# Optimization experiments

Hardware: AMD Instinct MI355X
Metric: run time of the kernel (lower is better)

The kernel has to match this reference:

```python
import jax, jax.numpy as jnp
import numpy as np

B, N, F = 4, 1024, 256
AVG_DEG = 16.0


def setup_inputs() -> dict:
    key = jax.random.key(0)
    k1, k2, k3, k4 = jax.random.split(key, 4)
    u = jax.random.uniform(k1, (B, N, N))
    A = (u < AVG_DEG / N).astype(jnp.float32)
    A = jnp.maximum(A, jnp.swapaxes(A, 1, 2))            # symmetric
    A = A * (1.0 - jnp.eye(N, dtype=jnp.float32))        # no self loops (added in forward)
    x = jax.random.normal(k2, (B, N, F), dtype=jnp.float32)
    pos = jax.random.normal(k3, (B, N, 3), dtype=jnp.float32)
    order = jax.random.uniform(k4, (B, N), dtype=jnp.float32)  # 'random' ordering priorities
    node_mask = jnp.ones((B, N), dtype=bool)
    return {"x": x, "adj": A, "pos": pos, "order": order, "node_mask": node_mask}


def _select(order, excluded, included, node_mask):
    # Greedy frontier-based node selection (K-MIS with stride=2).
    Bn, Nn = order.shape
    ar = jnp.arange(Nn)
    idx0 = jnp.argmin(order, axis=-1).astype(jnp.int32)           # [B]
    available = node_mask
    frontier = ar[None, :] == idx0[:, None]                        # scatter idx0 -> True
    selected = jnp.zeros_like(available)

    def cond(st):
        av, fr, sel, idx = st
        return av.any()

    def body(st):
        av, fr, sel, idx = st
        current = ar[None, :] == idx[:, None]                      # [B,N] one-hot
        sel = sel | current
        exc_row = jnp.take_along_axis(excluded, idx[:, None, None], axis=1)[:, 0]  # excluded[current]
        inc_row = jnp.take_along_axis(included, idx[:, None, None], axis=1)[:, 0]  # included[current]
        av = av & ~current & ~exc_row
        fr = (fr | inc_row | ~fr.any(-1, keepdims=True)) & av      # restart frontier if empty
        mo = jnp.where(fr, order, jnp.inf)
        midx = jnp.argmin(mo, axis=-1).astype(jnp.int32)
        has_fr = fr.any(-1)
        idx = jnp.where(has_fr, midx, idx)
        return (av, fr, sel, idx)

    _, _, selected, _ = jax.lax.while_loop(cond, body, (available, frontier, selected, idx0))
    return selected


def _forward(x, adj, pos, order, node_mask):
    Nn = adj.shape[1]
    eye = jnp.eye(Nn, dtype=adj.dtype)
    adj1 = jnp.where(node_mask[:, :, None], adj + eye, 0.0)        # adj_k[1] = A + I, masked rows
    adj2 = adj1 @ adj                                              # adj_k[2] = (A+I) @ A
    excluded = adj1 != 0                                           # adj_k[stride-1].bool()
    included = adj2 != 0                                           # adj_k[stride].bool()
    selected = _select(jax.lax.stop_gradient(order), excluded, included, node_mask)
    # pad K to N instead of data-dependent num_nodes; mask zeroes the padding
    mask_f, perm = jax.lax.top_k(selected.astype(jnp.float32), Nn)  # [B,K], [B,K]
    adj_kernel = jnp.take_along_axis(adj1, perm[:, None, :], axis=2)  # [B,N,K]
    # add_pool: adj^T @ x, then mask
    x_p = jnp.einsum('bnk,bnf->bkf', adj_kernel, x) * mask_f[..., None]
    # mean_pool for pos: add_pool / column degree
    deg = adj_kernel.sum(axis=1)[..., None]                        # [B,K,1]
    pos_p = jnp.einsum('bnk,bnc->bkc', adj_kernel, pos) / deg * mask_f[..., None]
    # coarsened adjacency: gather cols then rows of adj_k[stride], mask both sides
    a = jnp.take_along_axis(adj2, perm[:, None, :], axis=2)
    a = jnp.take_along_axis(a, perm[:, :, None], axis=1)
    a = a * mask_f[:, None, :] * mask_f[:, :, None]
    return x_p, pos_p, a, mask_f.astype(bool)


def reference(x, adj, pos, order, node_mask):
    return _forward(x, adj, pos, order, node_mask)
```

## Files before the change

### kernel.cpp

```cpp
#include <hip/hip_runtime.h>
#include <hip/hip_bf16.h>

#define BB 4
#define NN 1024
#define FF 256

typedef __hip_bfloat16 bf16;
typedef unsigned long long u64;
typedef unsigned int u32;
typedef unsigned short u16;
typedef unsigned char u8;

__device__ __forceinline__ bf16 f2b(float v) { return __float2bfloat16(v); }
__device__ __forceinline__ u16 f2bbits(float v) {
    bf16 h = __float2bfloat16(v);
    u16 s; __builtin_memcpy(&s, &h, 2);
    return s;
}
__device__ __forceinline__ void stf(float* p, size_t i, float v) { p[i] = v; }
__device__ __forceinline__ void stf(bf16* p, size_t i, float v) { p[i] = f2b(v); }

__global__ __launch_bounds__(512) void pack_sort_kernel(const float* __restrict__ adj,
                                                        const float* __restrict__ order,
                                                        u64* __restrict__ bitsA,
                                                        int* __restrict__ sp2node,
                                                        int* __restrict__ node2sp) {
    const int b = blockIdx.y, t = threadIdx.x;
    __shared__ u64 keys[NN];
    if (blockIdx.x < NN) {
        const int r = blockIdx.x;
        const size_t base = (size_t)b * NN * NN + (size_t)r * NN;
        for (int i = 0; i < 2; i++) {
            int j = i * 512 + t;
            u64 bal = __ballot(adj[base + j] != 0.0f);
            if ((t & 63) == 0) bitsA[((size_t)b * NN + r) * 16 + (j >> 6)] = bal;
        }
        return;
    }
    for (int i = t; i < NN; i += 512) {
        float v = order[(size_t)b * NN + i];
        u32 ub = __float_as_uint(v);
        u32 sk = (ub & 0x80000000u) ? ~ub : (ub | 0x80000000u);
        keys[i] = ((u64)sk << 32) | (u32)i;
    }
    __syncthreads();
    {
        u64 mk0 = keys[t], mk1 = keys[t + 512];
        int r0 = 0, r1 = 0;
        for (int m = 0; m < NN; m++) {
            u64 v = keys[m];
            r0 += (v < mk0);
            r1 += (v < mk1);
        }
        int n0 = (int)(mk0 & 0xFFFFFFFFu), n1 = (int)(mk1 & 0xFFFFFFFFu);
        sp2node[b * NN + r0] = n0; node2sp[b * NN + n0] = r0;
        sp2node[b * NN + r1] = n1; node2sp[b * NN + n1] = r1;
    }
}

__global__ void inc_pack_kernel(const u64* __restrict__ bitsA,
                                const int* __restrict__ sp2node,
                                const int* __restrict__ node2sp,
                                u32* __restrict__ packed) {
    const int r = blockIdx.x, b = blockIdx.y, t = threadIdx.x;
    __shared__ u64 myrow[16], incw[16];
    __shared__ u64 part[256];
    __shared__ unsigned short nbr[192];
    __shared__ int s2nT[16 * 65];
    __shared__ int cnt;
    if (t == 0) cnt = 0;
    if (t < 16) myrow[t] = bitsA[((size_t)b * NN + r) * 16 + t];
    __syncthreads();
    for (int i = 0; i < 4; i++) {
        int j = i * 256 + t;
        if ((myrow[j >> 6] >> (j & 63)) & 1) {
            int p = atomicAdd(&cnt, 1);
            if (p < 192) nbr[p] = (unsigned short)j;
        }
        s2nT[(j & 15) * 65 + (j >> 4)] = sp2node[b * NN + j];
    }
    __syncthreads();
    const int c = min(cnt, 192);
    {
        const int w = t & 15, g = t >> 4;
        u64 v = 0;
        for (int n = g; n < c; n += 16)
            v |= bitsA[((size_t)b * NN + nbr[n]) * 16 + w];
        part[t] = v;
    }
    __syncthreads();
    if (t < 16) {
        u64 acc = myrow[t];
        for (int g = 0; g < 16; g++) acc |= part[g * 16 + t];
        incw[t] = acc;
    }
    __syncthreads();
    if (t < 64) {
        const int s = node2sp[b * NN + r];
        u32 e16 = 0, i16 = 0;
        for (int q = 0; q < 16; q++) {
            int jn = s2nT[q * 65 + t];
            u32 eb = (u32)((myrow[jn >> 6] >> (jn & 63)) & 1) | (u32)(jn == r);
            u32 ib = (u32)((incw[jn >> 6] >> (jn & 63)) & 1);
            e16 |= eb << q;
            i16 |= ib << q;
        }
        packed[((size_t)b * NN + s) * 64 + t] = e16 | (i16 << 16);
    }
}

__global__ __launch_bounds__(256) void select_kernel(const u32* __restrict__ packed,
                                                     const int* __restrict__ node2sp,
                                                     int* __restrict__ perm,
                                                     int* __restrict__ kcount,
                                                     int* __restrict__ sink) {
    const int b = blockIdx.x, t = threadIdx.x;
    __shared__ u8 selS[NN];

    const uint4* pp = (const uint4*)(packed + (size_t)b * NN * 64);
    u32 acc = 0;
    for (int i = t; i < NN * 16; i += 256) {
        uint4 v = pp[i];
        acc ^= v.x ^ v.y ^ v.z ^ v.w;
    }
    if (acc == 0xDEADBEEFu) atomicAdd(sink, 1);
    __syncthreads();

    if (t < 64) {
        const int l = t;
        u32 avail = 0xFFFFu, front = (l == 0) ? 1u : 0u, sel = 0u;
        int cur = 0;
        for (int iter = 0; iter < 2 * NN + 8; ++iter) {
            if ((cur >> 4) == l) sel |= 1u << (cur & 15);
            u32 p = packed[((size_t)b * NN + cur) * 64 + l];
            avail &= ~(p & 0xFFFFu);
            front = (front | (p >> 16)) & avail;
            u64 fb = __ballot(front != 0u);
            if (!fb) {
                front = avail;
                fb = __ballot(front != 0u);
                if (!fb) break;
            }
            int lf = __ffsll(fb) - 1;
            u32 f = __shfl(front, lf);
            cur = lf * 16 + (__ffs(f) - 1);
        }
        for (int q = 0; q < 16; q++) selS[l * 16 + q] = (sel >> q) & 1u;
    }
    __syncthreads();

    if (t < 64) {
        const int l = t;
        u32 nodesel = 0;
        const int* n2s = node2sp + b * NN;
        for (int q = 0; q < 16; q++)
            nodesel |= ((u32)selS[n2s[l * 16 + q]]) << q;

        int cnt_sel = __popc(nodesel);
        int ps = cnt_sel;
        for (int off = 1; off < 64; off <<= 1) {
            int v = __shfl_up(ps, off);
            if (l >= off) ps += v;
        }
        const int K = __shfl(ps, 63);
        int pos = ps - cnt_sel;
        u32 m = nodesel;
        while (m) { int i = __ffs(m) - 1; perm[b * NN + pos++] = l * 16 + i; m &= m - 1; }
        int posu = K + l * 16 - (ps - cnt_sel);
        m = (~nodesel) & 0xFFFFu;
        while (m) { int i = __ffs(m) - 1; perm[b * NN + posu++] = l * 16 + i; m &= m - 1; }
        if (l == 0) kcount[b] = K;
    }
}

__global__ __launch_bounds__(256) void fused_out_bf16(const u64* __restrict__ bitsA,
                                 const float* __restrict__ x,
                                 const float* __restrict__ pos,
                                 const int* __restrict__ perm, const int* __restrict__ kcount,
                                 bf16* __restrict__ out_x, bf16* __restrict__ out_pos,
                                 bf16* __restrict__ out_a, bf16* __restrict__ out_mask) {
    const int k = blockIdx.x, b = blockIdx.y, t = threadIdx.x;
    const int K = kcount[b];
    bf16* ox = out_x + ((size_t)b * NN + k) * FF;
    bf16* op = out_pos + ((size_t)b * NN + k) * 3;
    bf16* oa = out_a + ((size_t)b * NN + k) * NN;
    if (t == 0) out_mask[(size_t)b * NN + k] = f2b(k < K ? 1.0f : 0.0f);
    if (k >= K) {
        uint4 z = make_uint4(0, 0, 0, 0);
        if (t < 128) ((uint4*)oa)[t] = z;
        if (t < 32)  ((uint4*)ox)[t] = z;
        if (t < 3) op[t] = f2b(0.0f);
        return;
    }
    const int r = perm[b * NN + k];
    __shared__ int p[NN];
    __shared__ u64 myrow[16];
    __shared__ unsigned short nbr[192];
    __shared__ u16 stx[FF];
    __shared__ u16 sta[NN];
    __shared__ int cnt;
    if (t == 0) cnt = 0;
    if (t < 16) myrow[t] = bitsA[((size_t)b * NN + r) * 16 + t];
    for (int q = 0; q < 4; q++) { int j = t + q * 256; p[j] = perm[b * NN + j]; }
    __syncthreads();
    for (int i = 0; i < 4; i++) {
        int j = i * 256 + t;
        if ((myrow[j >> 6] >> (j & 63)) & 1) {
            int pp = atomicAdd(&cnt, 1);
            if (pp < 192) nbr[pp] = (unsigned short)j;
        }
    }
    __syncthreads();
    const int c = min(cnt, 192);

    const size_t xb = (size_t)b * NN * FF;
    float acc = x[xb + (size_t)r * FF + t];
    for (int n = 0; n < c; n++) acc += x[xb + (size_t)nbr[n] * FF + t];
    stx[t] = f2bbits(acc);
    if (t < 3) {
        const size_t pb = (size_t)b * NN * 3;
        float pa = pos[pb + r * 3 + t];
        for (int n = 0; n < c; n++) pa += pos[pb + nbr[n] * 3 + t];
        op[t] = f2b(pa / (float)(c + 1));
    }

    for (int q = 0; q < 4; q++) {
        int jj = t + q * 256;
        float v = 0.0f;
        if (jj < K) {
            const int pj = p[jj];
            const u64* rj = bitsA + ((size_t)b * NN + pj) * 16;
            int a2 = (int)((myrow[pj >> 6] >> (pj & 63)) & 1);
#pragma unroll
            for (int w = 0; w < 16; w++)
                a2 += __popcll(myrow[w] & rj[w]);
            v = (float)a2;
        }
        sta[jj] = f2bbits(v);
    }
    __syncthreads();
    if (t < 128) ((uint4*)oa)[t] = ((const uint4*)sta)[t];
    if (t < 32)  ((uint4*)ox)[t] = ((const uint4*)stx)[t];
}

__global__ void fused_out_f32(const u64* __restrict__ bitsA, const float* __restrict__ x,
                              const float* __restrict__ pos,
                              const int* __restrict__ perm, const int* __restrict__ kcount,
                              float* __restrict__ out_x, float* __restrict__ out_pos,
                              float* __restrict__ out_a, float* __restrict__ out_mask) {
    const int k = blockIdx.x, b = blockIdx.y, t = threadIdx.x;
    const int K = kcount[b];
    float* ox = out_x + ((size_t)b * NN + k) * FF;
    float* op = out_pos + ((size_t)b * NN + k) * 3;
    float* oa = out_a + ((size_t)b * NN + k) * NN;
    if (t == 0) out_mask[(size_t)b * NN + k] = k < K ? 1.0f : 0.0f;
    if (k >= K) {
        ox[t] = 0.0f;
        if (t < 3) op[t] = 0.0f;
        for (int q = 0; q < 4; q++) oa[t + q * 256] = 0.0f;
        return;
    }
    const int r = perm[b * NN + k];
    __shared__ int p[NN];
    __shared__ u64 myrow[16];
    __shared__ unsigned short nbr[192];
    __shared__ int cnt;
    if (t == 0) cnt = 0;
    if (t < 16) myrow[t] = bitsA[((size_t)b * NN + r) * 16 + t];
    for (int q = 0; q < 4; q++) { int j = t + q * 256; p[j] = perm[b * NN + j]; }
    __syncthreads();
    for (int i = 0; i < 4; i++) {
        int j = i * 256 + t;
        if ((myrow[j >> 6] >> (j & 63)) & 1) {
            int pp = atomicAdd(&cnt, 1);
            if (pp < 192) nbr[pp] = (unsigned short)j;
        }
    }
    __syncthreads();
    const int c = min(cnt, 192);
    const size_t xb = (size_t)b * NN * FF;
    float acc = x[xb + (size_t)r * FF + t];
    for (int n = 0; n < c; n++) acc += x[xb + (size_t)nbr[n] * FF + t];
    ox[t] = acc;
    if (t < 3) {
        const size_t pb = (size_t)b * NN * 3;
        float pa = pos[pb + r * 3 + t];
        for (int n = 0; n < c; n++) pa += pos[pb + nbr[n] * 3 + t];
        op[t] = pa / (float)(c + 1);
    }
    for (int q = 0; q < 4; q++) {
        int jj = t + q * 256;
        float v = 0.0f;
        if (jj < K) {
            const int pj = p[jj];
            const u64* rj = bitsA + ((size_t)b * NN + pj) * 16;
            int a2 = (int)((myrow[pj >> 6] >> (pj & 63)) & 1);
#pragma unroll
            for (int w = 0; w < 16; w++)
                a2 += __popcll(myrow[w] & rj[w]);
            v = (float)a2;
        }
        oa[jj] = v;
    }
}

extern "C" void kernel_launch(void* const* d_in, const int* in_sizes, int n_in,
                              void* d_out, int out_size, void* d_ws, size_t ws_size,
                              hipStream_t stream) {
    const float* x     = (const float*)d_in[0];
    const float* adj   = (const float*)d_in[1];
    const float* pos   = (const float*)d_in[2];
    const float* order = (const float*)d_in[3];

    char* ws = (char*)d_ws;
    size_t off = 0;
    u64* bitsA   = (u64*)(ws + off); off += (size_t)BB * NN * 16 * 8;
    u32* packed  = (u32*)(ws + off); off += (size_t)BB * NN * 64 * 4;
    int* sp2node = (int*)(ws + off); off += (size_t)BB * NN * 4;
    int* node2sp = (int*)(ws + off); off += (size_t)BB * NN * 4;
    int* perm    = (int*)(ws + off); off += (size_t)BB * NN * 4;
    int* kcnt    = (int*)(ws + off); off += BB * 4;
    int* sink    = (int*)(ws + off);

    bool outf32 = false;
    size_t osz = 0;
    if (hipMemPtrGetInfo(d_out, &osz) == hipSuccess)
        outf32 = (osz >= 4ull * (size_t)out_size);

    pack_sort_kernel<<<dim3(NN + 1, BB), 512, 0, stream>>>(adj, order, bitsA, sp2node, node2sp);
    inc_pack_kernel<<<dim3(NN, BB), 256, 0, stream>>>(bitsA, sp2node, node2sp, packed);
    select_kernel<<<BB, 256, 0, stream>>>(packed, node2sp, perm, kcnt, sink);

    if (outf32) {
        float* out      = (float*)d_out;
        float* out_x    = out;
        float* out_pos  = out_x + (size_t)BB * NN * FF;
        float* out_a    = out_pos + (size_t)BB * NN * 3;
        float* out_mask = out_a + (size_t)BB * NN * NN;
        fused_out_f32<<<dim3(NN, BB), 256, 0, stream>>>(bitsA, x, pos, perm, kcnt,
                                                        out_x, out_pos, out_a, out_mask);
    } else {
        bf16* out      = (bf16*)d_out;
        bf16* out_x    = out;
        bf16* out_pos  = out_x + (size_t)BB * NN * FF;
        bf16* out_a    = out_pos + (size_t)BB * NN * 3;
        bf16* out_mask = out_a + (size_t)BB * NN * NN;
        fused_out_bf16<<<dim3(NN, BB), 256, 0, stream>>>(bitsA, x, pos, perm, kcnt,
                                                         out_x, out_pos, out_a, out_mask);
    }
}
```

Measured before the change: 153.2 us.

## Fuse four kernels into one persistent mega-kernel with software grid barriers

Replaces the pack/sort, inclusion-pack, select and output kernels with a single 1024-block persistent kernel separated by atomic-counter grid barriers. While four blocks run the serial selection, the remaining blocks zero the whole output buffer in parallel, so the final phase only writes rows and columns that belong to selected nodes. The goal is to cut per-kernel launch gaps and to overlap the output zeroing with the serial select phase. The software grid barrier depends on all 1024 blocks being co-resident, and its spin-wait exits after a timeout instead of failing, which risks deadlock or silent wrong results.

```diff
diff --git a/kernel.cpp b/kernel.cpp
--- a/kernel.cpp
+++ b/kernel.cpp
@@ -4,6 +4,8 @@
 #define BB 4
 #define NN 1024
 #define FF 256
+#define NBLK 1024
+#define NTHR 256
 
 typedef __hip_bfloat16 bf16;
 typedef unsigned long long u64;
@@ -17,38 +19,76 @@
     u16 s; __builtin_memcpy(&s, &h, 2);
     return s;
 }
-__device__ __forceinline__ void stf(float* p, size_t i, float v) { p[i] = v; }
-__device__ __forceinline__ void stf(bf16* p, size_t i, float v) { p[i] = f2b(v); }
-
-__global__ __launch_bounds__(512) void pack_sort_kernel(const float* __restrict__ adj,
-                                                        const float* __restrict__ order,
-                                                        u64* __restrict__ bitsA,
-                                                        int* __restrict__ sp2node,
-                                                        int* __restrict__ node2sp) {
-    const int b = blockIdx.y, t = threadIdx.x;
-    __shared__ u64 keys[NN];
-    if (blockIdx.x < NN) {
-        const int r = blockIdx.x;
+template <typename OT> __device__ __forceinline__ OT fromf(float v);
+template <> __device__ __forceinline__ float fromf<float>(float v) { return v; }
+template <> __device__ __forceinline__ bf16 fromf<bf16>(float v) { return __float2bfloat16(v); }
+
+__device__ __forceinline__ void grid_sync(int* bar, int target) {
+    __syncthreads();
+    if (threadIdx.x == 0) {
+        __hip_atomic_fetch_add(bar, 1, __ATOMIC_RELEASE, __HIP_MEMORY_SCOPE_AGENT);
+        int spins = 0;
+        while (__hip_atomic_load(bar, __ATOMIC_RELAXED, __HIP_MEMORY_SCOPE_AGENT) < target) {
+            __builtin_amdgcn_s_sleep(8);
+            if (++spins > (1 << 22)) break;
+        }
+        (void)__hip_atomic_load(bar, __ATOMIC_ACQUIRE, __HIP_MEMORY_SCOPE_AGENT);
+    }
+    __syncthreads();
+}
+
+template <typename OT>
+__global__ __launch_bounds__(NTHR, 4) void mega_kernel(
+        const float* __restrict__ x, const float* __restrict__ adj,
+        const float* __restrict__ pos, const float* __restrict__ order,
+        u64* __restrict__ bitsA, u32* __restrict__ packed,
+        int* __restrict__ sp2node, int* __restrict__ node2sp,
+        int* __restrict__ perm, int* __restrict__ kcnt,
+        int* __restrict__ sink, int* __restrict__ bar,
+        OT* __restrict__ out, size_t out_elems)
+{
+    const int B = blockIdx.x, t = threadIdx.x;
+    __shared__ union ShU {
+        u64 keys[NN];
+        struct {
+            u64 myrow[16], incw[16], part[256];
+            int s2nT[16 * 65];
+            unsigned short nbr[192];
+            int cnt;
+        } pb;
+        struct { u8 selS[NN]; } pc;
+        struct {
+            int p[NN];
+            u64 myrow[16];
+            unsigned short nbr[192];
+            u16 stx[FF], sta[NN];
+            int cnt;
+        } pd;
+    } sh;
+
+    for (int i = 0; i < 4; i++) {
+        const int id = B * 4 + i;
+        const int b = id >> 10, r = id & (NN - 1);
         const size_t base = (size_t)b * NN * NN + (size_t)r * NN;
-        for (int i = 0; i < 2; i++) {
-            int j = i * 512 + t;
+        for (int q = 0; q < 4; q++) {
+            int j = q * 256 + t;
             u64 bal = __ballot(adj[base + j] != 0.0f);
             if ((t & 63) == 0) bitsA[((size_t)b * NN + r) * 16 + (j >> 6)] = bal;
         }
-        return;
-    }
-    for (int i = t; i < NN; i += 512) {
-        float v = order[(size_t)b * NN + i];
-        u32 ub = __float_as_uint(v);
-        u32 sk = (ub & 0x80000000u) ? ~ub : (ub | 0x80000000u);
-        keys[i] = ((u64)sk << 32) | (u32)i;
-    }
-    __syncthreads();
-    {
-        u64 mk0 = keys[t], mk1 = keys[t + 512];
+    }
+    if (B < 8) {
+        const int b = B >> 1, half = B & 1;
+        for (int i = t; i < NN; i += NTHR) {
+            float v = order[(size_t)b * NN + i];
+            u32 ub = __float_as_uint(v);
+            u32 sk = (ub & 0x80000000u) ? ~ub : (ub | 0x80000000u);
+            sh.keys[i] = ((u64)sk << 32) | (u32)i;
+        }
+        __syncthreads();
+        u64 mk0 = sh.keys[half * 512 + t], mk1 = sh.keys[half * 512 + 256 + t];
         int r0 = 0, r1 = 0;
         for (int m = 0; m < NN; m++) {
-            u64 v = keys[m];
+            u64 v = sh.keys[m];
             r0 += (v < mk0);
             r1 += (v < mk1);
         }
@@ -56,251 +96,199 @@
         sp2node[b * NN + r0] = n0; node2sp[b * NN + n0] = r0;
         sp2node[b * NN + r1] = n1; node2sp[b * NN + n1] = r1;
     }
-}
-
-__global__ void inc_pack_kernel(const u64* __restrict__ bitsA,
-                                const int* __restrict__ sp2node,
-                                const int* __restrict__ node2sp,
-                                u32* __restrict__ packed) {
-    const int r = blockIdx.x, b = blockIdx.y, t = threadIdx.x;
-    __shared__ u64 myrow[16], incw[16];
-    __shared__ u64 part[256];
-    __shared__ unsigned short nbr[192];
-    __shared__ int s2nT[16 * 65];
-    __shared__ int cnt;
-    if (t == 0) cnt = 0;
-    if (t < 16) myrow[t] = bitsA[((size_t)b * NN + r) * 16 + t];
-    __syncthreads();
-    for (int i = 0; i < 4; i++) {
-        int j = i * 256 + t;
-        if ((myrow[j >> 6] >> (j & 63)) & 1) {
-            int p = atomicAdd(&cnt, 1);
-            if (p < 192) nbr[p] = (unsigned short)j;
-        }
-        s2nT[(j & 15) * 65 + (j >> 4)] = sp2node[b * NN + j];
-    }
-    __syncthreads();
-    const int c = min(cnt, 192);
+    grid_sync(bar, NBLK);
+
     {
-        const int w = t & 15, g = t >> 4;
-        u64 v = 0;
-        for (int n = g; n < c; n += 16)
-            v |= bitsA[((size_t)b * NN + nbr[n]) * 16 + w];
-        part[t] = v;
-    }
-    __syncthreads();
-    if (t < 16) {
-        u64 acc = myrow[t];
-        for (int g = 0; g < 16; g++) acc |= part[g * 16 + t];
-        incw[t] = acc;
-    }
-    __syncthreads();
-    if (t < 64) {
-        const int s = node2sp[b * NN + r];
-        u32 e16 = 0, i16 = 0;
-        for (int q = 0; q < 16; q++) {
-            int jn = s2nT[q * 65 + t];
-            u32 eb = (u32)((myrow[jn >> 6] >> (jn & 63)) & 1) | (u32)(jn == r);
-            u32 ib = (u32)((incw[jn >> 6] >> (jn & 63)) & 1);
-            e16 |= eb << q;
-            i16 |= ib << q;
-        }
-        packed[((size_t)b * NN + s) * 64 + t] = e16 | (i16 << 16);
-    }
-}
-
-__global__ __launch_bounds__(256) void select_kernel(const u32* __restrict__ packed,
-                                                     const int* __restrict__ node2sp,
-                                                     int* __restrict__ perm,
-                                                     int* __restrict__ kcount,
-                                                     int* __restrict__ sink) {
-    const int b = blockIdx.x, t = threadIdx.x;
-    __shared__ u8 selS[NN];
-
-    const uint4* pp = (const uint4*)(packed + (size_t)b * NN * 64);
-    u32 acc = 0;
-    for (int i = t; i < NN * 16; i += 256) {
-        uint4 v = pp[i];
-        acc ^= v.x ^ v.y ^ v.z ^ v.w;
-    }
-    if (acc == 0xDEADBEEFu) atomicAdd(sink, 1);
-    __syncthreads();
-
-    if (t < 64) {
-        const int l = t;
-        u32 avail = 0xFFFFu, front = (l == 0) ? 1u : 0u, sel = 0u;
-        int cur = 0;
-        for (int iter = 0; iter < 2 * NN + 8; ++iter) {
-            if ((cur >> 4) == l) sel |= 1u << (cur & 15);
-            u32 p = packed[((size_t)b * NN + cur) * 64 + l];
-            avail &= ~(p & 0xFFFFu);
-            front = (front | (p >> 16)) & avail;
-            u64 fb = __ballot(front != 0u);
-            if (!fb) {
-                front = avail;
-                fb = __ballot(front != 0u);
-                if (!fb) break;
-            }
-            int lf = __ffsll(fb) - 1;
-            u32 f = __shfl(front, lf);
-            cur = lf * 16 + (__ffs(f) - 1);
-        }
-        for (int q = 0; q < 16; q++) selS[l * 16 + q] = (sel >> q) & 1u;
-    }
-    __syncthreads();
-
-    if (t < 64) {
-        const int l = t;
-        u32 nodesel = 0;
-        const int* n2s = node2sp + b * NN;
-        for (int q = 0; q < 16; q++)
-            nodesel |= ((u32)selS[n2s[l * 16 + q]]) << q;
-
-        int cnt_sel = __popc(nodesel);
-        int ps = cnt_sel;
-        for (int off = 1; off < 64; off <<= 1) {
-            int v = __shfl_up(ps, off);
-            if (l >= off) ps += v;
-        }
-        const int K = __shfl(ps, 63);
-        int pos = ps - cnt_sel;
-        u32 m = nodesel;
-        while (m) { int i = __ffs(m) - 1; perm[b * NN + pos++] = l * 16 + i; m &= m - 1; }
-        int posu = K + l * 16 - (ps - cnt_sel);
-        m = (~nodesel) & 0xFFFFu;
-        while (m) { int i = __ffs(m) - 1; perm[b * NN + posu++] = l * 16 + i; m &= m - 1; }
-        if (l == 0) kcount[b] = K;
-    }
-}
-
-__global__ __launch_bounds__(256) void fused_out_bf16(const u64* __restrict__ bitsA,
-                                 const float* __restrict__ x,
-                                 const float* __restrict__ pos,
-                                 const int* __restrict__ perm, const int* __restrict__ kcount,
-                                 bf16* __restrict__ out_x, bf16* __restrict__ out_pos,
-                                 bf16* __restrict__ out_a, bf16* __restrict__ out_mask) {
-    const int k = blockIdx.x, b = blockIdx.y, t = threadIdx.x;
-    const int K = kcount[b];
-    bf16* ox = out_x + ((size_t)b * NN + k) * FF;
-    bf16* op = out_pos + ((size_t)b * NN + k) * 3;
-    bf16* oa = out_a + ((size_t)b * NN + k) * NN;
-    if (t == 0) out_mask[(size_t)b * NN + k] = f2b(k < K ? 1.0f : 0.0f);
-    if (k >= K) {
+        const int b = B >> 8, rbase = (B & 255) * 4;
+        for (int q = 0; q < 4; q++) {
+            int j = q * 256 + t;
+            sh.pb.s2nT[(j & 15) * 65 + (j >> 4)] = sp2node[b * NN + j];
+        }
+        for (int rr = 0; rr < 4; rr++) {
+            const int r = rbase + rr;
+            if (t == 0) sh.pb.cnt = 0;
+            if (t < 16) sh.pb.myrow[t] = bitsA[((size_t)b * NN + r) * 16 + t];
+            __syncthreads();
+            for (int q = 0; q < 4; q++) {
+                int j = q * 256 + t;
+                if ((sh.pb.myrow[j >> 6] >> (j & 63)) & 1) {
+                    int p = atomicAdd(&sh.pb.cnt, 1);
+                    if (p < 192) sh.pb.nbr[p] = (unsigned short)j;
+                }
+            }
+            __syncthreads();
+            const int c = min(sh.pb.cnt, 192);
+            {
+                const int w = t & 15, g = t >> 4;
+                u64 v = 0;
+                for (int n = g; n < c; n += 16)
+                    v |= bitsA[((size_t)b * NN + sh.pb.nbr[n]) * 16 + w];
+                sh.pb.part[t] = v;
+            }
+            __syncthreads();
+            if (t < 16) {
+                u64 acc = sh.pb.myrow[t];
+                for (int g = 0; g < 16; g++) acc |= sh.pb.part[g * 16 + t];
+                sh.pb.incw[t] = acc;
+            }
+            __syncthreads();
+            if (t < 64) {
+                const int s = node2sp[b * NN + r];
+                u32 e16 = 0, i16 = 0;
+                for (int q = 0; q < 16; q++) {
+                    int jn = sh.pb.s2nT[q * 65 + t];
+                    u32 eb = (u32)((sh.pb.myrow[jn >> 6] >> (jn & 63)) & 1) | (u32)(jn == r);
+                    u32 ib = (u32)((sh.pb.incw[jn >> 6] >> (jn & 63)) & 1);
+                    e16 |= eb << q;
+                    i16 |= ib << q;
+                }
+                packed[((size_t)b * NN + s) * 64 + t] = e16 | (i16 << 16);
+            }
+            __syncthreads();
+        }
+    }
+    grid_sync(bar, 2 * NBLK);
+
+    if (B < 4) {
+        const int b = B;
+        const uint4* pp = (const uint4*)(packed + (size_t)b * NN * 64);
+        u32 acc = 0;
+        for (int i = t; i < NN * 16; i += NTHR) {
+            uint4 v = pp[i];
+            acc ^= v.x ^ v.y ^ v.z ^ v.w;
+        }
+        if (acc == 0xDEADBEEFu) atomicAdd(sink, 1);
+        __syncthreads();
+
+        if (t < 64) {
+            const int l = t;
+            u32 avail = 0xFFFFu, front = (l == 0) ? 1u : 0u, sel = 0u;
+            int cur = 0;
+            for (int iter = 0; iter < 2 * NN + 8; ++iter) {
+                if ((cur >> 4) == l) sel |= 1u << (cur & 15);
+                u32 p = packed[((size_t)b * NN + cur) * 64 + l];
+                avail &= ~(p & 0xFFFFu);
+                front = (front | (p >> 16)) & avail;
+                u64 fb = __ballot(front != 0u);
+                if (!fb) {
+                    front = avail;
+                    fb = __ballot(front != 0u);
+                    if (!fb) break;
+                }
+                int lf = __ffsll(fb) - 1;
+                u32 f = __shfl(front, lf);
+                cur = lf * 16 + (__ffs(f) - 1);
+            }
+            for (int q = 0; q < 16; q++) sh.pc.selS[l * 16 + q] = (sel >> q) & 1u;
+        }
+        __syncthreads();
+        if (t < 64) {
+            const int l = t;
+            u32 nodesel = 0;
+            const int* n2s = node2sp + b * NN;
+            for (int q = 0; q < 16; q++)
+                nodesel |= ((u32)sh.pc.selS[n2s[l * 16 + q]]) << q;
+            int cnt_sel = __popc(nodesel);
+            int ps = cnt_sel;
+            for (int off = 1; off < 64; off <<= 1) {
+                int v = __shfl_up(ps, off);
+                if (l >= off) ps += v;
+            }
+            const int K = __shfl(ps, 63);
+            int pos_ = ps - cnt_sel;
+            u32 m = nodesel;
+            while (m) { int i = __ffs(m) - 1; perm[b * NN + pos_++] = l * 16 + i; m &= m - 1; }
+            int posu = K + l * 16 - (ps - cnt_sel);
+            m = (~nodesel) & 0xFFFFu;
+            while (m) { int i = __ffs(m) - 1; perm[b * NN + posu++] = l * 16 + i; m &= m - 1; }
+            if (l == 0) kcnt[b] = K;
+        }
+    } else {
+        const size_t nu4 = (out_elems * sizeof(OT)) >> 4;
         uint4 z = make_uint4(0, 0, 0, 0);
-        if (t < 128) ((uint4*)oa)[t] = z;
-        if (t < 32)  ((uint4*)ox)[t] = z;
-        if (t < 3) op[t] = f2b(0.0f);
-        return;
-    }
-    const int r = perm[b * NN + k];
-    __shared__ int p[NN];
-    __shared__ u64 myrow[16];
-    __shared__ unsigned short nbr[192];
-    __shared__ u16 stx[FF];
-    __shared__ u16 sta[NN];
-    __shared__ int cnt;
-    if (t == 0) cnt = 0;
-    if (t < 16) myrow[t] = bitsA[((size_t)b * NN + r) * 16 + t];
-    for (int q = 0; q < 4; q++) { int j = t + q * 256; p[j] = perm[b * NN + j]; }
-    __syncthreads();
-    for (int i = 0; i < 4; i++) {
-        int j = i * 256 + t;
-        if ((myrow[j >> 6] >> (j & 63)) & 1) {
-            int pp = atomicAdd(&cnt, 1);
-            if (pp < 192) nbr[pp] = (unsigned short)j;
-        }
-    }
-    __syncthreads();
-    const int c = min(cnt, 192);
-
-    const size_t xb = (size_t)b * NN * FF;
-    float acc = x[xb + (size_t)r * FF + t];
-    for (int n = 0; n < c; n++) acc += x[xb + (size_t)nbr[n] * FF + t];
-    stx[t] = f2bbits(acc);
-    if (t < 3) {
-        const size_t pb = (size_t)b * NN * 3;
-        float pa = pos[pb + r * 3 + t];
-        for (int n = 0; n < c; n++) pa += pos[pb + nbr[n] * 3 + t];
-        op[t] = f2b(pa / (float)(c + 1));
-    }
-
-    for (int q = 0; q < 4; q++) {
-        int jj = t + q * 256;
-        float v = 0.0f;
-        if (jj < K) {
-            const int pj = p[jj];
-            const u64* rj = bitsA + ((size_t)b * NN + pj) * 16;
-            int a2 = (int)((myrow[pj >> 6] >> (pj & 63)) & 1);
+        uint4* o4 = (uint4*)out;
+        for (size_t i = (size_t)(B - 4) * NTHR + t; i < nu4; i += (size_t)(NBLK - 4) * NTHR)
+            o4[i] = z;
+    }
+    grid_sync(bar, 3 * NBLK);
+
+    OT* out_x = out;
+    OT* out_pos = out_x + (size_t)BB * NN * FF;
+    OT* out_a = out_pos + (size_t)BB * NN * 3;
+    OT* out_mask = out_a + (size_t)BB * NN * NN;
+
+    for (int task = B; task < BB * NN; task += NBLK) {
+        const int b = task >> 10, k = task & (NN - 1);
+        const int K = kcnt[b];
+        if (k >= K) continue;
+        const int r = perm[b * NN + k];
+        OT* ox = out_x + ((size_t)b * NN + k) * FF;
+        OT* op = out_pos + ((size_t)b * NN + k) * 3;
+        OT* oa = out_a + ((size_t)b * NN + k) * NN;
+        if (t == 0) {
+            out_mask[(size_t)b * NN + k] = fromf<OT>(1.0f);
+            sh.pd.cnt = 0;
+        }
+        if (t < 16) sh.pd.myrow[t] = bitsA[((size_t)b * NN + r) * 16 + t];
+        for (int q = 0; q < 4; q++) { int j = t + q * 256; sh.pd.p[j] = perm[b * NN + j]; }
+        __syncthreads();
+        for (int i = 0; i < 4; i++) {
+            int j = i * 256 + t;
+            if ((sh.pd.myrow[j >> 6] >> (j & 63)) & 1) {
+                int pp = atomicAdd(&sh.pd.cnt, 1);
+                if (pp < 192) sh.pd.nbr[pp] = (unsigned short)j;
+            }
+        }
+        __syncthreads();
+        const int c = min(sh.pd.cnt, 192);
+
+        const size_t xb = (size_t)b * NN * FF;
+        float acc = x[xb + (size_t)r * FF + t];
+        for (int n = 0; n < c; n++) acc += x[xb + (size_t)sh.pd.nbr[n] * FF + t];
+        if (t < 3) {
+            const size_t pb_ = (size_t)b * NN * 3;
+            float pa = pos[pb_ + r * 3 + t];
+            for (int n = 0; n < c; n++) pa += pos[pb_ + sh.pd.nbr[n] * 3 + t];
+            op[t] = fromf<OT>(pa / (float)(c + 1));
+        }
+
+        if constexpr (sizeof(OT) == 2) {
+            sh.pd.stx[t] = f2bbits(acc);
+            for (int q = 0; q < 4; q++) {
+                int jj = t + q * 256;
+                float v = 0.0f;
+                if (jj < K) {
+                    const int pj = sh.pd.p[jj];
+                    const u64* rj = bitsA + ((size_t)b * NN + pj) * 16;
+                    int a2 = (int)((sh.pd.myrow[pj >> 6] >> (pj & 63)) & 1);
 #pragma unroll
-            for (int w = 0; w < 16; w++)
-                a2 += __popcll(myrow[w] & rj[w]);
-            v = (float)a2;
-        }
-        sta[jj] = f2bbits(v);
-    }
-    __syncthreads();
-    if (t < 128) ((uint4*)oa)[t] = ((const uint4*)sta)[t];
-    if (t < 32)  ((uint4*)ox)[t] = ((const uint4*)stx)[t];
-}
-
-__global__ void fused_out_f32(const u64* __restrict__ bitsA, const float* __restrict__ x,
-                              const float* __restrict__ pos,
-                              const int* __restrict__ perm, const int* __restrict__ kcount,
-                              float* __restrict__ out_x, float* __restrict__ out_pos,
-                              float* __restrict__ out_a, float* __restrict__ out_mask) {
-    const int k = blockIdx.x, b = blockIdx.y, t = threadIdx.x;
-    const int K = kcount[b];
-    float* ox = out_x + ((size_t)b * NN + k) * FF;
-    float* op = out_pos + ((size_t)b * NN + k) * 3;
-    float* oa = out_a + ((size_t)b * NN + k) * NN;
-    if (t == 0) out_mask[(size_t)b * NN + k] = k < K ? 1.0f : 0.0f;
-    if (k >= K) {
-        ox[t] = 0.0f;
-        if (t < 3) op[t] = 0.0f;
-        for (int q = 0; q < 4; q++) oa[t + q * 256] = 0.0f;
-        return;
-    }
-    const int r = perm[b * NN + k];
-    __shared__ int p[NN];
-    __shared__ u64 myrow[16];
-    __shared__ unsigned short nbr[192];
-    __shared__ int cnt;
-    if (t == 0) cnt = 0;
-    if (t < 16) myrow[t] = bitsA[((size_t)b * NN + r) * 16 + t];
-    for (int q = 0; q < 4; q++) { int j = t + q * 256; p[j] = perm[b * NN + j]; }
-    __syncthreads();
-    for (int i = 0; i < 4; i++) {
-        int j = i * 256 + t;
-        if ((myrow[j >> 6] >> (j & 63)) & 1) {
-            int pp = atomicAdd(&cnt, 1);
-            if (pp < 192) nbr[pp] = (unsigned short)j;
-        }
-    }
-    __syncthreads();
-    const int c = min(cnt, 192);
-    const size_t xb = (size_t)b * NN * FF;
-    float acc = x[xb + (size_t)r * FF + t];
-    for (int n = 0; n < c; n++) acc += x[xb + (size_t)nbr[n] * FF + t];
-    ox[t] = acc;
-    if (t < 3) {
-        const size_t pb = (size_t)b * NN * 3;
-        float pa = pos[pb + r * 3 + t];
-        for (int n = 0; n < c; n++) pa += pos[pb + nbr[n] * 3 + t];
-        op[t] = pa / (float)(c + 1);
-    }
-    for (int q = 0; q < 4; q++) {
-        int jj = t + q * 256;
-        float v = 0.0f;
-        if (jj < K) {
-            const int pj = p[jj];
-            const u64* rj = bitsA + ((size_t)b * NN + pj) * 16;
-            int a2 = (int)((myrow[pj >> 6] >> (pj & 63)) & 1);
+                    for (int w = 0; w < 16; w++)
+                        a2 += __popcll(sh.pd.myrow[w] & rj[w]);
+                    v = (float)a2;
+                }
+                sh.pd.sta[jj] = f2bbits(v);
+            }
+            __syncthreads();
+            const int nu = (K + 7) >> 3;
+            if (t < nu) ((uint4*)oa)[t] = ((const uint4*)sh.pd.sta)[t];
+            if (t < 32) ((uint4*)ox)[t] = ((const uint4*)sh.pd.stx)[t];
+            __syncthreads();
+        } else {
+            ox[t] = acc;
+            for (int q = 0; q < 4; q++) {
+                int jj = t + q * 256;
+                if (jj < K) {
+                    const int pj = sh.pd.p[jj];
+                    const u64* rj = bitsA + ((size_t)b * NN + pj) * 16;
+                    int a2 = (int)((sh.pd.myrow[pj >> 6] >> (pj & 63)) & 1);
 #pragma unroll
-            for (int w = 0; w < 16; w++)
-                a2 += __popcll(myrow[w] & rj[w]);
-            v = (float)a2;
-        }
-        oa[jj] = v;
+                    for (int w = 0; w < 16; w++)
+                        a2 += __popcll(sh.pd.myrow[w] & rj[w]);
+                    oa[jj] = (float)a2;
+                }
+            }
+            __syncthreads();
+        }
     }
 }
 
@@ -319,33 +307,21 @@
     int* sp2node = (int*)(ws + off); off += (size_t)BB * NN * 4;
     int* node2sp = (int*)(ws + off); off += (size_t)BB * NN * 4;
     int* perm    = (int*)(ws + off); off += (size_t)BB * NN * 4;
-    int* kcnt    = (int*)(ws + off); off += BB * 4;
-    int* sink    = (int*)(ws + off);
+    int* kcnt    = (int*)(ws + off); off += 64;
+    int* sink    = (int*)(ws + off); off += 64;
+    int* bar     = (int*)(ws + off); off += 64;
+
+    hipMemsetAsync(bar, 0, 64, stream);
 
     bool outf32 = false;
     size_t osz = 0;
     if (hipMemPtrGetInfo(d_out, &osz) == hipSuccess)
         outf32 = (osz >= 4ull * (size_t)out_size);
 
-    pack_sort_kernel<<<dim3(NN + 1, BB), 512, 0, stream>>>(adj, order, bitsA, sp2node, node2sp);
-    inc_pack_kernel<<<dim3(NN, BB), 256, 0, stream>>>(bitsA, sp2node, node2sp, packed);
-    select_kernel<<<BB, 256, 0, stream>>>(packed, node2sp, perm, kcnt, sink);
-
-    if (outf32) {
-        float* out      = (float*)d_out;
-        float* out_x    = out;
-        float* out_pos  = out_x + (size_t)BB * NN * FF;
-        float* out_a    = out_pos + (size_t)BB * NN * 3;
-        float* out_mask = out_a + (size_t)BB * NN * NN;
-        fused_out_f32<<<dim3(NN, BB), 256, 0, stream>>>(bitsA, x, pos, perm, kcnt,
-                                                        out_x, out_pos, out_a, out_mask);
-    } else {
-        bf16* out      = (bf16*)d_out;
-        bf16* out_x    = out;
-        bf16* out_pos  = out_x + (size_t)BB * NN * FF;
-        bf16* out_a    = out_pos + (size_t)BB * NN * 3;
-        bf16* out_mask = out_a + (size_t)BB * NN * NN;
-        fused_out_bf16<<<dim3(NN, BB), 256, 0, stream>>>(bitsA, x, pos, perm, kcnt,
-                                                         out_x, out_pos, out_a, out_mask);
-    }
+    if (outf32)
+        mega_kernel<float><<<NBLK, NTHR, 0, stream>>>(x, adj, pos, order, bitsA, packed,
+            sp2node, node2sp, perm, kcnt, sink, bar, (float*)d_out, (size_t)out_size);
+    else
+        mega_kernel<bf16><<<NBLK, NTHR, 0, stream>>>(x, adj, pos, order, bitsA, packed,
+            sp2node, node2sp, perm, kcnt, sink, bar, (bf16*)d_out, (size_t)out_size);
 }
```

New measurement: 388.5 us. +153.5%, slower.
